# Kernel tuning notes

Hardware: AMD Instinct MI355X
Metric: run time of the kernel (lower is better)

## Reference

```python
import jax, jax.numpy as jnp
import numpy as np

B_, L_ = 8, 2048            # batch, seq_len
AD, VD, H = 512, 512, 256    # audio_dim, visual_dim, hidden_dim (= mamba d_model)
EXPAND, DSTATE, DCONV = 2, 16, 4
DIN = EXPAND * H             # mamba d_inner = 512
DTRANK = (H + 15) // 16      # ceil(d_model/16) = 16
NCLS = 8


def setup_inputs() -> dict:
    key = jax.random.key(0)
    ks = jax.random.split(key, 16)
    w = lambda k, shape, s=0.02: jax.random.normal(k, shape, jnp.float32) * s
    return {
        "audio_feats": jax.random.normal(ks[0], (B_, L_, AD), jnp.float32),
        "visual_feats": jax.random.normal(ks[1], (B_, L_, VD), jnp.float32),
        "audio_w": w(ks[2], (H, AD)), "audio_b": jnp.zeros((H,), jnp.float32),
        "visual_w": w(ks[3], (H, VD)), "visual_b": jnp.zeros((H,), jnp.float32),
        "q_w": w(ks[4], (H, H)), "q_b": jnp.zeros((H,), jnp.float32),
        "k_w": w(ks[5], (H, H)), "k_b": jnp.zeros((H,), jnp.float32),
        "v_w": w(ks[6], (H, H)), "v_b": jnp.zeros((H,), jnp.float32),
        "in_proj_w": w(ks[7], (2 * DIN, H)),
        "conv_w": w(ks[8], (DIN, DCONV), 0.1), "conv_b": jnp.zeros((DIN,), jnp.float32),
        "x_proj_w": w(ks[9], (DTRANK + 2 * DSTATE, DIN)),
        "dt_proj_w": w(ks[10], (DIN, DTRANK), 0.1),
        "dt_proj_b": jnp.full((DIN,), -4.0, jnp.float32),  # softplus(-4) ~ small dt
        "A_log": jnp.log(jnp.tile(jnp.arange(1, DSTATE + 1, dtype=jnp.float32), (DIN, 1))),
        "D": jnp.ones((DIN,), jnp.float32),
        "out_proj_w": w(ks[11], (H, DIN)),
        "cls_w": w(ks[12], (NCLS, H)), "cls_b": jnp.zeros((NCLS,), jnp.float32),
    }


def _linear(x, w, b):
    return jnp.einsum('...i,oi->...o', x, w) + b


def _mamba(u, in_proj_w, conv_w, conv_b, x_proj_w, dt_proj_w, dt_proj_b, A_log, D, out_proj_w):
    # u: [B, L, d_model]
    xz = jnp.einsum('bld,ed->ble', u, in_proj_w)          # [B, L, 2*DIN]
    x, z = jnp.split(xz, 2, axis=-1)
    # causal depthwise conv1d (torch pads d_conv-1 both sides then truncates to L)
    lhs = jnp.swapaxes(x, 1, 2)                            # [B, DIN, L]
    rhs = conv_w[:, None, :]                               # [DIN, 1, DCONV]
    xc = jax.lax.conv_general_dilated(lhs, rhs, (1,), [(DCONV - 1, 0)],
                                      feature_group_count=DIN)
    x = jax.nn.silu(jnp.swapaxes(xc, 1, 2) + conv_b)       # [B, L, DIN]
    dbc = jnp.einsum('bld,ed->ble', x, x_proj_w)           # [B, L, DTRANK+2*DSTATE]
    dt, Bm, Cm = jnp.split(dbc, [DTRANK, DTRANK + DSTATE], axis=-1)
    dt = jax.nn.softplus(jnp.einsum('blr,dr->bld', dt, dt_proj_w) + dt_proj_b)
    A = -jnp.exp(A_log)                                    # [DIN, DSTATE]

    def step(h, inputs):
        dt_t, B_t, C_t, x_t = inputs                       # [B,DIN],[B,DSTATE],[B,DSTATE],[B,DIN]
        dA = jnp.exp(dt_t[:, :, None] * A)                 # [B, DIN, DSTATE]
        h = dA * h + (dt_t * x_t)[:, :, None] * B_t[:, None, :]
        y = jnp.einsum('bds,bs->bd', h, C_t)
        return h, y

    h0 = jnp.zeros((u.shape[0], DIN, DSTATE), x.dtype)
    xs = (jnp.swapaxes(dt, 0, 1), jnp.swapaxes(Bm, 0, 1),
          jnp.swapaxes(Cm, 0, 1), jnp.swapaxes(x, 0, 1))
    _, ys = jax.lax.scan(step, h0, xs)                     # ys: [L, B, DIN]
    y = jnp.swapaxes(ys, 0, 1) + x * D
    y = y * jax.nn.silu(z)
    return jnp.einsum('bld,od->blo', y, out_proj_w)        # [B, L, d_model]


def reference(audio_feats, visual_feats, audio_w, audio_b, visual_w, visual_b,
              q_w, q_b, k_w, k_b, v_w, v_b, in_proj_w, conv_w, conv_b,
              x_proj_w, dt_proj_w, dt_proj_b, A_log, D, out_proj_w, cls_w, cls_b):
    ah = _linear(audio_feats, audio_w, audio_b)            # [B, L, H]
    vh = _linear(visual_feats, visual_w, visual_b)         # [B, L, H]
    Q = _linear(ah, q_w, q_b)
    K = _linear(vh, k_w, k_b)
    V = _linear(vh, v_w, v_b)
    scores = jnp.einsum('bqd,bkd->bqk', Q, K) / jnp.sqrt(jnp.float32(H))
    attn = jax.nn.softmax(scores, axis=-1)                 # [B, L, L]
    fused = jnp.einsum('bqk,bkd->bqd', attn, V)            # [B, L, H]
    mo = _mamba(fused, in_proj_w, conv_w, conv_b, x_proj_w,
                dt_proj_w, dt_proj_b, A_log, D, out_proj_w)
    pooled = mo.mean(axis=1)                               # [B, H]
    logits = _linear(pooled, cls_w, cls_b)                 # [B, NCLS]
    preds = jax.nn.softmax(logits, axis=-1)
    return logits, preds
```

## Files before the change

kernel.cpp:

```cpp
#include <hip/hip_runtime.h>
#include <hip/hip_bf16.h>
#include <math.h>

#define B_    8
#define L_    2048
#define AD    512
#define VD    512
#define H_    256
#define DIN   512
#define DSTATE 16
#define DCONV  4
#define DTRANK 16
#define NCLS   8
#define BL    (B_ * L_)
#define NCH   64
#define CLEN  32
#define NSP   4

typedef __attribute__((ext_vector_type(8))) short bf16x8;
typedef __attribute__((ext_vector_type(4))) float f32x4;

__global__ __launch_bounds__(256)
void cast_bf16_kernel(const float* __restrict__ src, __hip_bfloat16* __restrict__ dst)
{
    size_t i = ((size_t)blockIdx.x * 256 + threadIdx.x) * 8;
    float4 a = *(const float4*)(src + i);
    float4 b = *(const float4*)(src + i + 4);
    bf16x8 o;
    __hip_bfloat16 t;
    t = __float2bfloat16(a.x); o[0] = *(short*)&t;
    t = __float2bfloat16(a.y); o[1] = *(short*)&t;
    t = __float2bfloat16(a.z); o[2] = *(short*)&t;
    t = __float2bfloat16(a.w); o[3] = *(short*)&t;
    t = __float2bfloat16(b.x); o[4] = *(short*)&t;
    t = __float2bfloat16(b.y); o[5] = *(short*)&t;
    t = __float2bfloat16(b.z); o[6] = *(short*)&t;
    t = __float2bfloat16(b.w); o[7] = *(short*)&t;
    *(bf16x8*)(dst + i) = o;
}

__global__ __launch_bounds__(256)
void cast_weights_kernel(const float* __restrict__ qw, const float* __restrict__ kw,
                         const float* __restrict__ vw, const float* __restrict__ ipw,
                         const float* __restrict__ xpw,
                         __hip_bfloat16* __restrict__ qwb, __hip_bfloat16* __restrict__ kwb,
                         __hip_bfloat16* __restrict__ vwb, __hip_bfloat16* __restrict__ ipwb,
                         __hip_bfloat16* __restrict__ xpwb)
{
    size_t i = ((size_t)blockIdx.x * 256 + threadIdx.x) * 8;
    const float* s; __hip_bfloat16* d; size_t off;
    if      (i <  65536) { s = qw;  d = qwb;  off = i; }
    else if (i < 131072) { s = kw;  d = kwb;  off = i - 65536; }
    else if (i < 196608) { s = vw;  d = vwb;  off = i - 131072; }
    else if (i < 458752) { s = ipw; d = ipwb; off = i - 196608; }
    else                 { s = xpw; d = xpwb; off = i - 458752; }
    float4 a = *(const float4*)(s + off);
    float4 b = *(const float4*)(s + off + 4);
    bf16x8 o;
    __hip_bfloat16 t;
    t = __float2bfloat16(a.x); o[0] = *(short*)&t;
    t = __float2bfloat16(a.y); o[1] = *(short*)&t;
    t = __float2bfloat16(a.z); o[2] = *(short*)&t;
    t = __float2bfloat16(a.w); o[3] = *(short*)&t;
    t = __float2bfloat16(b.x); o[4] = *(short*)&t;
    t = __float2bfloat16(b.y); o[5] = *(short*)&t;
    t = __float2bfloat16(b.z); o[6] = *(short*)&t;
    t = __float2bfloat16(b.w); o[7] = *(short*)&t;
    *(bf16x8*)(d + off) = o;
}

__global__ __launch_bounds__(256)
void transpose_wT_kernel(const float* __restrict__ aw, const float* __restrict__ vw,
                         __hip_bfloat16* __restrict__ awT, __hip_bfloat16* __restrict__ vwT)
{
    int i = blockIdx.x * 256 + threadIdx.x;
    const float* s = (i < 131072) ? aw : vw;
    __hip_bfloat16* d = (i < 131072) ? awT : vwT;
    int j = i & 131071;
    int r = j >> 9;
    int c = j & 511;
    d[c * 256 + r] = __float2bfloat16(s[j]);
}

__global__ __launch_bounds__(256)
void bias_compose_kernel(const float* __restrict__ qw, const float* __restrict__ kw,
                         const float* __restrict__ vw,
                         const float* __restrict__ ab, const float* __restrict__ vb,
                         const float* __restrict__ qb, const float* __restrict__ kb,
                         const float* __restrict__ vb2,
                         float* __restrict__ bq, float* __restrict__ bkv)
{
    int m = threadIdx.x;
    int seg = blockIdx.x;
    const float* w  = (seg == 0) ? qw : (seg == 1) ? kw : vw;
    const float* ib = (seg == 0) ? ab : vb;
    const float* ob = (seg == 0) ? qb : (seg == 1) ? kb : vb2;
    float s = ob[m];
    for (int i = 0; i < 256; ++i) s += w[m * 256 + i] * ib[i];
    if (seg == 0) bq[m] = s;
    else          bkv[(seg - 1) * 256 + m] = s;
}

template<int N, int K, int OBF>
__global__ __launch_bounds__(64, 2)
void gemm_mfma_t(const __hip_bfloat16* __restrict__ A,
                 const __hip_bfloat16* __restrict__ W,
                 const float* __restrict__ bias,
                 void* __restrict__ outp)
{
    const int lane = threadIdx.x;
    const int l15  = lane & 15;
    const int quad = lane >> 4;
    const int m0   = blockIdx.x * 16;
    const int n0   = blockIdx.y * 64;

    const __hip_bfloat16* Arow = A + (size_t)(m0 + l15) * K + quad * 8;
    f32x4 acc[4];
    #pragma unroll
    for (int nt = 0; nt < 4; ++nt) acc[nt] = (f32x4){0.f, 0.f, 0.f, 0.f};

    #pragma unroll
    for (int kc = 0; kc < K; kc += 32) {
        bf16x8 af = *(const bf16x8*)(Arow + kc);
        #pragma unroll
        for (int nt = 0; nt < 4; ++nt) {
            bf16x8 bfv = *(const bf16x8*)(W + (size_t)(n0 + nt * 16 + l15) * K + kc + quad * 8);
            acc[nt] = __builtin_amdgcn_mfma_f32_16x16x32_bf16(af, bfv, acc[nt], 0, 0, 0);
        }
    }
    #pragma unroll
    for (int nt = 0; nt < 4; ++nt) {
        int col = n0 + nt * 16 + l15;
        float bv = bias ? bias[col] : 0.f;
        #pragma unroll
        for (int r = 0; r < 4; ++r) {
            size_t idx = (size_t)(m0 + quad * 4 + r) * N + col;
            float v = acc[nt][r] + bv;
            if (OBF) ((__hip_bfloat16*)outp)[idx] = __float2bfloat16(v);
            else     ((float*)outp)[idx] = v;
        }
    }
}

template<int N, int K, int NT, int OBF, int ACT>
__global__ __launch_bounds__(256, 2)
void gemm4_t(const __hip_bfloat16* __restrict__ A,
             const __hip_bfloat16* __restrict__ W,
             const float* __restrict__ bias,
             void* __restrict__ outp)
{
    constexpr int NROWS = NT * 16;
    __shared__ __attribute__((aligned(16))) short Ws[NROWS * 264];
    const int tid  = threadIdx.x;
    const int lane = tid & 63;
    const int w    = tid >> 6;
    const int l15  = lane & 15;
    const int quad = lane >> 4;
    const int m0   = blockIdx.x * 64 + w * 16;
    const int n0   = blockIdx.y * 64;

    constexpr int KC = K / 32;
    bf16x8 af[KC];
    const __hip_bfloat16* Arow = A + (size_t)(m0 + l15) * K + quad * 8;
    #pragma unroll
    for (int kc = 0; kc < KC; ++kc) af[kc] = *(const bf16x8*)(Arow + kc * 32);

    f32x4 acc[NT];
    #pragma unroll
    for (int nt = 0; nt < NT; ++nt) acc[nt] = (f32x4){0.f, 0.f, 0.f, 0.f};

    #pragma unroll
    for (int kh = 0; kh < K / 256; ++kh) {
        __syncthreads();
        #pragma unroll
        for (int i = 0; i < 8; ++i) {
            int id = tid + i * 256;
            int row = id >> 5, c = id & 31;
            if (row < NROWS)
                *(bf16x8*)&Ws[row * 264 + c * 8] =
                    *(const bf16x8*)(W + (size_t)(n0 + row) * K + kh * 256 + c * 8);
        }
        __syncthreads();
        #pragma unroll
        for (int kc = 0; kc < 8; ++kc) {
            #pragma unroll
            for (int nt = 0; nt < NT; ++nt) {
                bf16x8 wv = *(const bf16x8*)&Ws[(nt * 16 + l15) * 264 + kc * 32 + quad * 8];
                acc[nt] = __builtin_amdgcn_mfma_f32_16x16x32_bf16(af[kh * 8 + kc], wv, acc[nt], 0, 0, 0);
            }
        }
    }
    #pragma unroll
    for (int nt = 0; nt < NT; ++nt) {
        int col = n0 + nt * 16 + l15;
        float bv = bias ? bias[col] : 0.f;
        #pragma unroll
        for (int r = 0; r < 4; ++r) {
            size_t idx = (size_t)(m0 + quad * 4 + r) * N + col;
            float v = acc[nt][r] + bv;
            if (ACT) v = v / (1.f + __expf(-v));
            if (OBF) ((__hip_bfloat16*)outp)[idx] = __float2bfloat16(v);
            else     ((float*)outp)[idx] = v;
        }
    }
}

__global__ __launch_bounds__(256)
void transpose_v_kernel(const __hip_bfloat16* __restrict__ KV,
                        __hip_bfloat16* __restrict__ Vt)
{
    const int tid = threadIdx.x;
    const int lc  = blockIdx.x & 7;
    const int hg  = (blockIdx.x >> 3) & 31;
    const int b   = blockIdx.x >> 8;
    const int l   = lc * 256 + tid;
    bf16x8 v = *(const bf16x8*)(KV + ((size_t)b * L_ + l) * 512 + 256 + hg * 8);
    __hip_bfloat16* dst = Vt + (size_t)b * H_ * L_ + (size_t)(hg * 8) * L_ + l;
    #pragma unroll
    for (int j = 0; j < 8; ++j) {
        short s = v[j];
        dst[(size_t)j * L_] = *(__hip_bfloat16*)&s;
    }
}

__global__ __launch_bounds__(256, 3)
void attn_split_kernel(const __hip_bfloat16* __restrict__ Q,
                       const __hip_bfloat16* __restrict__ KV,
                       const __hip_bfloat16* __restrict__ Vt,
                       __hip_bfloat16* __restrict__ Opart,
                       float* __restrict__ lpart)
{
    __shared__ __attribute__((aligned(16))) short Ks[32 * 264];
    __shared__ __attribute__((aligned(16))) short Vs[256 * 40];
    __shared__ __attribute__((aligned(16))) short Pls[4][16 * 40];

    const int tid  = threadIdx.x;
    const int lane = tid & 63;
    const int w    = tid >> 6;
    const int b    = blockIdx.x & 7;
    const int qt   = (blockIdx.x >> 3) & 31;
    const int sp   = blockIdx.x >> 8;
    const int q0   = qt * 64 + w * 16;
    const int l15  = lane & 15;
    const int quad = lane >> 4;

    const __hip_bfloat16* Qb = Q  + ((size_t)b * L_ + q0) * H_;
    const __hip_bfloat16* Kb = KV + (size_t)b * L_ * 512;
    const __hip_bfloat16* Vb = Vt + (size_t)b * H_ * L_;

    bf16x8 qf[8];
    #pragma unroll
    for (int kc = 0; kc < 8; ++kc)
        qf[kc] = *(const bf16x8*)(Qb + (size_t)l15 * H_ + kc * 32 + quad * 8);

    f32x4 Oacc[16];
    #pragma unroll
    for (int nt = 0; nt < 16; ++nt) Oacc[nt] = (f32x4){0.f, 0.f, 0.f, 0.f};
    float lsum[4] = {0.f, 0.f, 0.f, 0.f};

    const int kbase = sp * 512;
    for (int st = 0; st < 16; ++st) {
        const int kb = kbase + st * 32;
        bf16x8 kreg[4], vreg[4];
        #pragma unroll
        for (int i = 0; i < 4; ++i) {
            int id = tid + i * 256;
            int row = id >> 5, c16 = id & 31;
            kreg[i] = *(const bf16x8*)(Kb + (size_t)(kb + row) * 512 + c16 * 8);
        }
        #pragma unroll
        for (int i = 0; i < 4; ++i) {
            int id = tid + i * 256;
            int row = id >> 2, c = id & 3;
            vreg[i] = *(const bf16x8*)(Vb + (size_t)row * L_ + kb + c * 8);
        }
        __syncthreads();
        #pragma unroll
        for (int i = 0; i < 4; ++i) {
            int id = tid + i * 256;
            int row = id >> 5, c16 = id & 31;
            *(bf16x8*)&Ks[row * 264 + c16 * 8] = kreg[i];
        }
        #pragma unroll
        for (int i = 0; i < 4; ++i) {
            int id = tid + i * 256;
            int row = id >> 2, c = id & 3;
            *(bf16x8*)&Vs[row * 40 + c * 8] = vreg[i];
        }
        __syncthreads();
        f32x4 S[2];
        #pragma unroll
        for (int nt = 0; nt < 2; ++nt) {
            S[nt] = (f32x4){0.f, 0.f, 0.f, 0.f};
            #pragma unroll
            for (int kc = 0; kc < 8; ++kc) {
                bf16x8 bk = *(const bf16x8*)&Ks[(nt * 16 + l15) * 264 + kc * 32 + quad * 8];
                S[nt] = __builtin_amdgcn_mfma_f32_16x16x32_bf16(qf[kc], bk, S[nt], 0, 0, 0);
            }
        }
        #pragma unroll
        for (int nt = 0; nt < 2; ++nt)
            #pragma unroll
            for (int r = 0; r < 4; ++r) {
                float p = __expf(S[nt][r] * 0.0625f);
                lsum[r] += p;
                __hip_bfloat16 pb = __float2bfloat16(p);
                Pls[w][(quad * 4 + r) * 40 + nt * 16 + l15] = *(short*)&pb;
            }
        bf16x8 pf = *(const bf16x8*)&Pls[w][l15 * 40 + quad * 8];
        #pragma unroll
        for (int nt = 0; nt < 16; ++nt) {
            bf16x8 vf = *(const bf16x8*)&Vs[(nt * 16 + l15) * 40 + quad * 8];
            Oacc[nt] = __builtin_amdgcn_mfma_f32_16x16x32_bf16(pf, vf, Oacc[nt], 0, 0, 0);
        }
    }
    #pragma unroll
    for (int r = 0; r < 4; ++r) {
        lsum[r] += __shfl_xor(lsum[r], 1, 64);
        lsum[r] += __shfl_xor(lsum[r], 2, 64);
        lsum[r] += __shfl_xor(lsum[r], 4, 64);
        lsum[r] += __shfl_xor(lsum[r], 8, 64);
    }
    __hip_bfloat16* Ob = Opart + (((size_t)sp * B_ + b) * L_ + q0) * H_;
    #pragma unroll
    for (int r = 0; r < 4; ++r)
        #pragma unroll
        for (int nt = 0; nt < 16; ++nt)
            Ob[(size_t)(quad * 4 + r) * H_ + nt * 16 + l15] = __float2bfloat16(Oacc[nt][r]);
    if (l15 == 0) {
        #pragma unroll
        for (int r = 0; r < 4; ++r)
            lpart[((size_t)sp * B_ + b) * L_ + q0 + quad * 4 + r] = lsum[r];
    }
}

__global__ __launch_bounds__(256)
void attn_merge_kernel(const __hip_bfloat16* __restrict__ Opart,
                       const float* __restrict__ lpart,
                       __hip_bfloat16* __restrict__ O)
{
    const size_t idx = (size_t)blockIdx.x * 256 + threadIdx.x;
    const size_t row = idx >> 8;
    float o = 0.f, l = 0.f;
    #pragma unroll
    for (int sp = 0; sp < NSP; ++sp) {
        o += __bfloat162float(Opart[(size_t)sp * BL * H_ + idx]);
        l += lpart[(size_t)sp * BL + row];
    }
    O[idx] = __float2bfloat16(o / l);
}

__global__ __launch_bounds__(256)
void conv_silu_kernel(const float* __restrict__ xb,
                      const float* __restrict__ cw,
                      const float* __restrict__ cb,
                      float* __restrict__ xconv,
                      __hip_bfloat16* __restrict__ xconvbf)
{
    const int idx = blockIdx.x * 256 + threadIdx.x;
    const int d = idx & (DIN - 1);
    const int l = (idx >> 9) & (L_ - 1);
    const int b = idx >> 20;
    float acc = cb[d];
    #pragma unroll
    for (int j = 0; j < DCONV; ++j) {
        int ls = l - (DCONV - 1) + j;
        if (ls >= 0) acc += xb[((size_t)b * L_ + ls) * DIN + d] * cw[d * DCONV + j];
    }
    float sg = 1.f / (1.f + __expf(-acc));
    float v = acc * sg;
    xconv[(size_t)idx] = v;
    xconvbf[(size_t)idx] = __float2bfloat16(v);
}

__global__ __launch_bounds__(256)
void scan_p1_kernel(const float* __restrict__ xconv,
                    const float* __restrict__ zw,
                    const float* __restrict__ dbc,
                    const float* __restrict__ dtw,
                    const float* __restrict__ dtbias,
                    const float* __restrict__ A_log,
                    const float* __restrict__ Dv,
                    float* __restrict__ hend,
                    float* __restrict__ aprod,
                    float* __restrict__ Gbuf,
                    float* __restrict__ accloc)
{
    __shared__ float Ds[CLEN][16];
    __shared__ float Bs[CLEN][16];
    __shared__ float Cs[CLEN][16];
    const int tid  = threadIdx.x;
    const int dgrp = blockIdx.x & 1;
    const int c    = (blockIdx.x >> 1) & 63;
    const int b    = blockIdx.x >> 7;
    const int d    = dgrp * 256 + tid;
    const size_t rbase = (size_t)b * L_ + c * CLEN;

    for (int i = tid; i < CLEN * 16; i += 256) {
        int tl = i >> 4, s = i & 15;
        Ds[tl][s] = dbc[(rbase + tl) * 48 + s];
        Bs[tl][s] = dbc[(rbase + tl) * 48 + 16 + s];
        Cs[tl][s] = dbc[(rbase + tl) * 48 + 32 + s];
    }
    __syncthreads();

    float wr[16];
    #pragma unroll
    for (int r = 0; r < 16; ++r) wr[r] = dtw[d * DTRANK + r];
    const float dbias = dtbias[d];
    const float Dval  = Dv[d];

    float Aa[16];
    bool fast = true;
    #pragma unroll
    for (int s = 0; s < 16; ++s) {
        Aa[s] = -__expf(A_log[d * DSTATE + s]);
        fast = fast && (fabsf(Aa[s] + (float)(s + 1)) < 1e-3f);
    }

    float h[16], ap[16], g[16];
    #pragma unroll
    for (int s = 0; s < 16; ++s) { h[s] = 0.f; ap[s] = 1.f; g[s] = 0.f; }
    float acc = 0.f;

    if (fast) {
        for (int t = 0; t < CLEN; ++t) {
            float d0 = dbias, d1 = 0.f;
            #pragma unroll
            for (int r = 0; r < 8; ++r) { d0 += Ds[t][r] * wr[r]; d1 += Ds[t][r + 8] * wr[r + 8]; }
            float dot = d0 + d1;
            float dtv = (dot > 20.f) ? dot : __logf(1.f + __expf(dot));
            float xv  = xconv[(rbase + t) * DIN + d];
            float wt  = zw   [(rbase + t) * DIN + d];
            float u  = dtv * xv;
            float e1 = __expf(-dtv);
            float ep = 1.f;
            #pragma unroll
            for (int s = 0; s < 16; ++s) {
                ep *= e1;
                ap[s] *= ep;
                h[s] = ep * h[s] + u * Bs[t][s];
                float tc = wt * Cs[t][s];
                acc += tc * h[s];
                g[s] += tc * ap[s];
            }
            acc += wt * xv * Dval;
        }
    } else {
        for (int t = 0; t < CLEN; ++t) {
            float d0 = dbias, d1 = 0.f;
            #pragma unroll
            for (int r = 0; r < 8; ++r) { d0 += Ds[t][r] * wr[r]; d1 += Ds[t][r + 8] * wr[r + 8]; }
            float dot = d0 + d1;
            float dtv = (dot > 20.f) ? dot : __logf(1.f + __expf(dot));
            float xv  = xconv[(rbase + t) * DIN + d];
            float wt  = zw   [(rbase + t) * DIN + d];
            float u  = dtv * xv;
            #pragma unroll
            for (int s = 0; s < 16; ++s) {
                float e = __expf(dtv * Aa[s]);
                ap[s] *= e;
                h[s] = e * h[s] + u * Bs[t][s];
                float tc = wt * Cs[t][s];
                acc += tc * h[s];
                g[s] += tc * ap[s];
            }
            acc += wt * xv * Dval;
        }
    }
    size_t o = (((size_t)b * NCH + c) * DIN + d) * 16;
    #pragma unroll
    for (int s = 0; s < 16; ++s) { hend[o + s] = h[s]; aprod[o + s] = ap[s]; Gbuf[o + s] = g[s]; }
    accloc[((size_t)b * NCH + c) * DIN + d] = acc;
}

__global__ __launch_bounds__(256)
void scan_p2_kernel(const float* __restrict__ hend,
                    const float* __restrict__ aprod,
                    const float* __restrict__ Gbuf,
                    const float* __restrict__ accloc,
                    float* __restrict__ ybar)
{
    const int g  = blockIdx.x * 256 + threadIdx.x;
    const int b  = g >> 13;
    const int ds = g & 8191;
    const int d  = ds >> 4;
    const int s  = ds & 15;
    float h = 0.f, part = 0.f;
    for (int c = 0; c < NCH; ++c) {
        size_t idx = (((size_t)b * NCH + c) << 13) + ds;
        part += Gbuf[idx] * h;
        h = aprod[idx] * h + hend[idx];
    }
    part += __shfl_xor(part, 1, 64);
    part += __shfl_xor(part, 2, 64);
    part += __shfl_xor(part, 4, 64);
    part += __shfl_xor(part, 8, 64);
    if (s == 0) {
        float a = 0.f;
        for (int c = 0; c < NCH; ++c)
            a += accloc[((size_t)b * NCH + c) * DIN + d];
        ybar[b * DIN + d] = (part + a) * (1.f / (float)L_);
    }
}

__global__ __launch_bounds__(256)
void head_kernel(const float* __restrict__ ybar,
                 const float* __restrict__ opw,
                 const float* __restrict__ clsw,
                 const float* __restrict__ clsb,
                 float* __restrict__ out)
{
    __shared__ float pooled_s[H_];
    __shared__ float logit_s[NCLS];
    const int tid = threadIdx.x;
    const int b   = blockIdx.x;
    const float* yb = ybar + b * DIN;
    const float* wr = opw + (size_t)tid * DIN;
    float p = 0.f;
    for (int dd = 0; dd < DIN; dd += 4) {
        float4 y4 = *(const float4*)(yb + dd);
        float4 w4 = *(const float4*)(wr + dd);
        p += y4.x*w4.x + y4.y*w4.y + y4.z*w4.z + y4.w*w4.w;
    }
    pooled_s[tid] = p;
    __syncthreads();
    if (tid < NCLS) {
        float lg = clsb[tid];
        const float* cw = clsw + tid * H_;
        for (int hh = 0; hh < H_; ++hh) lg += pooled_s[hh] * cw[hh];
        logit_s[tid] = lg;
        out[b * NCLS + tid] = lg;
    }
    __syncthreads();
    if (tid == 0) {
        float mx = logit_s[0];
        for (int c = 1; c < NCLS; ++c) mx = fmaxf(mx, logit_s[c]);
        float ssum = 0.f; float e[NCLS];
        for (int c = 0; c < NCLS; ++c) { e[c] = __expf(logit_s[c] - mx); ssum += e[c]; }
        for (int c = 0; c < NCLS; ++c) out[B_*NCLS + b * NCLS + c] = e[c] / ssum;
    }
}

extern "C" void kernel_launch(void* const* d_in, const int* in_sizes, int n_in,
                              void* d_out, int out_size, void* d_ws, size_t ws_size,
                              hipStream_t stream)
{
    const float* audio    = (const float*)d_in[0];
    const float* visual   = (const float*)d_in[1];
    const float* audio_w  = (const float*)d_in[2];
    const float* audio_b  = (const float*)d_in[3];
    const float* visual_w = (const float*)d_in[4];
    const float* visual_b = (const float*)d_in[5];
    const float* q_w = (const float*)d_in[6];
    const float* q_b = (const float*)d_in[7];
    const float* k_w = (const float*)d_in[8];
    const float* k_b = (const float*)d_in[9];
    const float* v_w = (const float*)d_in[10];
    const float* v_b = (const float*)d_in[11];
    const float* in_proj_w = (const float*)d_in[12];
    const float* conv_w    = (const float*)d_in[13];
    const float* conv_b    = (const float*)d_in[14];
    const float* x_proj_w  = (const float*)d_in[15];
    const float* dt_proj_w = (const float*)d_in[16];
    const float* dt_proj_b = (const float*)d_in[17];
    const float* A_log     = (const float*)d_in[18];
    const float* Dvec      = (const float*)d_in[19];
    const float* out_proj_w= (const float*)d_in[20];
    const float* cls_w     = (const float*)d_in[21];
    const float* cls_b     = (const float*)d_in[22];
    float* out = (float*)d_out;
    float* ws  = (float*)d_ws;

    __hip_bfloat16* abf  = (__hip_bfloat16*)(ws);
    __hip_bfloat16* vbf  = (__hip_bfloat16*)(ws + 4194304);
    __hip_bfloat16* Qbf  = (__hip_bfloat16*)(ws + 8388608);
    __hip_bfloat16* KVbf = (__hip_bfloat16*)(ws + 10485760);
    __hip_bfloat16* Vt   = (__hip_bfloat16*)(ws + 14680064);
    __hip_bfloat16* fusedbf = (__hip_bfloat16*)(ws + 16777216);
    __hip_bfloat16* Opart   = (__hip_bfloat16*)(ws + 18874368);
    float* xbuf  = ws;
    float* zw    = ws + 8388608;
    float* xconv = ws + 18874368;
    __hip_bfloat16* xconvbf = (__hip_bfloat16*)(ws + 27262976);
    float* hend   = ws;
    float* aprod  = ws + 4194304;
    float* Gbuf   = ws + 27262976;
    float* accloc = ws + 16777216;
    float* ybar   = ws + 17039360;
    __hip_bfloat16* q_wbf   = (__hip_bfloat16*)(ws + 31457280);
    __hip_bfloat16* k_wbf   = (__hip_bfloat16*)(ws + 31490048);
    __hip_bfloat16* v_wbf   = (__hip_bfloat16*)(ws + 31522816);
    __hip_bfloat16* ipwbf   = (__hip_bfloat16*)(ws + 31555584);
    __hip_bfloat16* xpwbf   = (__hip_bfloat16*)(ws + 31686656);
    __hip_bfloat16* awT     = (__hip_bfloat16*)(ws + 31698944);
    __hip_bfloat16* vwT     = (__hip_bfloat16*)(ws + 31764480);
    __hip_bfloat16* Wqp     = (__hip_bfloat16*)(ws + 31830016);
    __hip_bfloat16* Wkvp    = (__hip_bfloat16*)(ws + 31895552);
    float* bq     = ws + 32026624;
    float* bkv    = ws + 32026880;
    float* lpart  = ws + 32027392;
    float* dbcb   = ws + 32092928;

    dim3 blk(256);
    cast_bf16_kernel<<<dim3(4096), blk, 0, stream>>>(audio,  abf);
    cast_bf16_kernel<<<dim3(4096), blk, 0, stream>>>(visual, vbf);
    cast_weights_kernel<<<dim3(236), blk, 0, stream>>>(q_w, k_w, v_w, in_proj_w, x_proj_w,
                                                       q_wbf, k_wbf, v_wbf, ipwbf, xpwbf);
    transpose_wT_kernel<<<dim3(1024), blk, 0, stream>>>(audio_w, visual_w, awT, vwT);
    gemm_mfma_t<512, 256, 1><<<dim3(16, 8), dim3(64), 0, stream>>>(q_wbf, awT, nullptr, Wqp);
    gemm_mfma_t<512, 256, 1><<<dim3(16, 8), dim3(64), 0, stream>>>(k_wbf, vwT, nullptr, Wkvp);
    gemm_mfma_t<512, 256, 1><<<dim3(16, 8), dim3(64), 0, stream>>>(v_wbf, vwT, nullptr, Wkvp + 256 * 512);
    bias_compose_kernel<<<dim3(3), blk, 0, stream>>>(q_w, k_w, v_w, audio_b, visual_b,
                                                     q_b, k_b, v_b, bq, bkv);
    gemm4_t<256, 512, 4, 1, 0><<<dim3(256, 4), blk, 0, stream>>>(abf, Wqp,  bq,  Qbf);
    gemm4_t<512, 512, 4, 1, 0><<<dim3(256, 8), blk, 0, stream>>>(vbf, Wkvp, bkv, KVbf);
    transpose_v_kernel<<<dim3(2048), blk, 0, stream>>>(KVbf, Vt);
    attn_split_kernel<<<dim3(1024), blk, 0, stream>>>(Qbf, KVbf, Vt, Opart, lpart);
    attn_merge_kernel<<<dim3(16384), blk, 0, stream>>>(Opart, lpart, fusedbf);
    gemm4_t<512, 256, 4, 0, 0><<<dim3(256, 8), blk, 0, stream>>>(fusedbf, ipwbf,           nullptr, xbuf);
    gemm4_t<512, 256, 4, 0, 1><<<dim3(256, 8), blk, 0, stream>>>(fusedbf, ipwbf + DIN*H_,  nullptr, zw);
    conv_silu_kernel<<<dim3(BL*DIN/256), blk, 0, stream>>>(xbuf, conv_w, conv_b, xconv, xconvbf);
    gemm4_t<48, 512, 3, 0, 0><<<dim3(256, 1), blk, 0, stream>>>(xconvbf, xpwbf, nullptr, dbcb);
    scan_p1_kernel<<<dim3(1024), blk, 0, stream>>>(xconv, zw, dbcb, dt_proj_w, dt_proj_b,
                                                   A_log, Dvec, hend, aprod, Gbuf, accloc);
    scan_p2_kernel<<<dim3(256), blk, 0, stream>>>(hend, aprod, Gbuf, accloc, ybar);
    head_kernel<<<dim3(8), blk, 0, stream>>>(ybar, out_proj_w, cls_w, cls_b, out);
}
```

Measured before the change: 467.9 us.

## Merge prep kernels, widen attention tiles, store Mamba intermediates in bf16, split scan combine

Several independent changes. The input and weight cast, transpose and bias kernels are merged into fewer launches, and the three composition GEMMs now run as one 3D-grid launch. Attention blocks now cover 128 query rows, with each wave handling two 16-row sets so every K/V tile loaded into shared memory is reused twice; occupancy is lowered to 2 blocks. The in_proj outputs and conv output are stored as bf16 instead of fp32 to halve memory traffic, at some cost in precision. The sequential cross-chunk scan combine is split into two stages (groups of 8 chunks, then 8 groups) to expose more parallelism.

```diff
diff --git a/kernel.cpp b/kernel.cpp
--- a/kernel.cpp
+++ b/kernel.cpp
@@ -16,18 +16,14 @@
 #define NCH   64
 #define CLEN  32
 #define NSP   4
+#define NGRP  8
 
 typedef __attribute__((ext_vector_type(8))) short bf16x8;
 typedef __attribute__((ext_vector_type(4))) float f32x4;
 
-__global__ __launch_bounds__(256)
-void cast_bf16_kernel(const float* __restrict__ src, __hip_bfloat16* __restrict__ dst)
-{
-    size_t i = ((size_t)blockIdx.x * 256 + threadIdx.x) * 8;
-    float4 a = *(const float4*)(src + i);
-    float4 b = *(const float4*)(src + i + 4);
-    bf16x8 o;
-    __hip_bfloat16 t;
+__device__ inline bf16x8 pack8(float4 a, float4 b)
+{
+    bf16x8 o; __hip_bfloat16 t;
     t = __float2bfloat16(a.x); o[0] = *(short*)&t;
     t = __float2bfloat16(a.y); o[1] = *(short*)&t;
     t = __float2bfloat16(a.z); o[2] = *(short*)&t;
@@ -36,109 +32,108 @@
     t = __float2bfloat16(b.y); o[5] = *(short*)&t;
     t = __float2bfloat16(b.z); o[6] = *(short*)&t;
     t = __float2bfloat16(b.w); o[7] = *(short*)&t;
-    *(bf16x8*)(dst + i) = o;
-}
-
-__global__ __launch_bounds__(256)
-void cast_weights_kernel(const float* __restrict__ qw, const float* __restrict__ kw,
-                         const float* __restrict__ vw, const float* __restrict__ ipw,
-                         const float* __restrict__ xpw,
-                         __hip_bfloat16* __restrict__ qwb, __hip_bfloat16* __restrict__ kwb,
-                         __hip_bfloat16* __restrict__ vwb, __hip_bfloat16* __restrict__ ipwb,
-                         __hip_bfloat16* __restrict__ xpwb)
+    return o;
+}
+
+__global__ __launch_bounds__(256)
+void cast_inputs_kernel(const float* __restrict__ a, const float* __restrict__ v,
+                        __hip_bfloat16* __restrict__ ab, __hip_bfloat16* __restrict__ vb)
 {
     size_t i = ((size_t)blockIdx.x * 256 + threadIdx.x) * 8;
     const float* s; __hip_bfloat16* d; size_t off;
-    if      (i <  65536) { s = qw;  d = qwb;  off = i; }
-    else if (i < 131072) { s = kw;  d = kwb;  off = i - 65536; }
-    else if (i < 196608) { s = vw;  d = vwb;  off = i - 131072; }
-    else if (i < 458752) { s = ipw; d = ipwb; off = i - 196608; }
-    else                 { s = xpw; d = xpwb; off = i - 458752; }
-    float4 a = *(const float4*)(s + off);
-    float4 b = *(const float4*)(s + off + 4);
-    bf16x8 o;
-    __hip_bfloat16 t;
-    t = __float2bfloat16(a.x); o[0] = *(short*)&t;
-    t = __float2bfloat16(a.y); o[1] = *(short*)&t;
-    t = __float2bfloat16(a.z); o[2] = *(short*)&t;
-    t = __float2bfloat16(a.w); o[3] = *(short*)&t;
-    t = __float2bfloat16(b.x); o[4] = *(short*)&t;
-    t = __float2bfloat16(b.y); o[5] = *(short*)&t;
-    t = __float2bfloat16(b.z); o[6] = *(short*)&t;
-    t = __float2bfloat16(b.w); o[7] = *(short*)&t;
-    *(bf16x8*)(d + off) = o;
-}
-
-__global__ __launch_bounds__(256)
-void transpose_wT_kernel(const float* __restrict__ aw, const float* __restrict__ vw,
-                         __hip_bfloat16* __restrict__ awT, __hip_bfloat16* __restrict__ vwT)
-{
-    int i = blockIdx.x * 256 + threadIdx.x;
-    const float* s = (i < 131072) ? aw : vw;
-    __hip_bfloat16* d = (i < 131072) ? awT : vwT;
-    int j = i & 131071;
-    int r = j >> 9;
-    int c = j & 511;
-    d[c * 256 + r] = __float2bfloat16(s[j]);
-}
-
-__global__ __launch_bounds__(256)
-void bias_compose_kernel(const float* __restrict__ qw, const float* __restrict__ kw,
-                         const float* __restrict__ vw,
-                         const float* __restrict__ ab, const float* __restrict__ vb,
-                         const float* __restrict__ qb, const float* __restrict__ kb,
-                         const float* __restrict__ vb2,
-                         float* __restrict__ bq, float* __restrict__ bkv)
-{
-    int m = threadIdx.x;
-    int seg = blockIdx.x;
-    const float* w  = (seg == 0) ? qw : (seg == 1) ? kw : vw;
-    const float* ib = (seg == 0) ? ab : vb;
-    const float* ob = (seg == 0) ? qb : (seg == 1) ? kb : vb2;
-    float s = ob[m];
-    for (int i = 0; i < 256; ++i) s += w[m * 256 + i] * ib[i];
-    if (seg == 0) bq[m] = s;
-    else          bkv[(seg - 1) * 256 + m] = s;
-}
-
-template<int N, int K, int OBF>
+    if (i < 8388608) { s = a; d = ab; off = i; }
+    else             { s = v; d = vb; off = i - 8388608; }
+    float4 x = *(const float4*)(s + off);
+    float4 y = *(const float4*)(s + off + 4);
+    *(bf16x8*)(d + off) = pack8(x, y);
+}
+
+__global__ __launch_bounds__(256)
+void prep_kernel(const float* __restrict__ qw, const float* __restrict__ kw,
+                 const float* __restrict__ vw, const float* __restrict__ ipw,
+                 const float* __restrict__ xpw,
+                 const float* __restrict__ aw, const float* __restrict__ vww,
+                 const float* __restrict__ ab, const float* __restrict__ vb,
+                 const float* __restrict__ qb, const float* __restrict__ kb,
+                 const float* __restrict__ vb2,
+                 __hip_bfloat16* __restrict__ qwb, __hip_bfloat16* __restrict__ kwb,
+                 __hip_bfloat16* __restrict__ vwb, __hip_bfloat16* __restrict__ ipwb,
+                 __hip_bfloat16* __restrict__ xpwb,
+                 __hip_bfloat16* __restrict__ awT, __hip_bfloat16* __restrict__ vwT,
+                 float* __restrict__ bq, float* __restrict__ bkv)
+{
+    const int blk = blockIdx.x;
+    if (blk < 236) {
+        size_t i = ((size_t)blk * 256 + threadIdx.x) * 8;
+        const float* s; __hip_bfloat16* d; size_t off;
+        if      (i <  65536) { s = qw;  d = qwb;  off = i; }
+        else if (i < 131072) { s = kw;  d = kwb;  off = i - 65536; }
+        else if (i < 196608) { s = vw;  d = vwb;  off = i - 131072; }
+        else if (i < 458752) { s = ipw; d = ipwb; off = i - 196608; }
+        else                 { s = xpw; d = xpwb; off = i - 458752; }
+        float4 x = *(const float4*)(s + off);
+        float4 y = *(const float4*)(s + off + 4);
+        *(bf16x8*)(d + off) = pack8(x, y);
+    } else if (blk < 1260) {
+        int i = (blk - 236) * 256 + threadIdx.x;
+        const float* s = (i < 131072) ? aw : vww;
+        __hip_bfloat16* d = (i < 131072) ? awT : vwT;
+        int j = i & 131071;
+        int r = j >> 9, c = j & 511;
+        d[c * 256 + r] = __float2bfloat16(s[j]);
+    } else {
+        int seg = blk - 1260;
+        int m = threadIdx.x;
+        const float* w  = (seg == 0) ? qw : (seg == 1) ? kw : vw;
+        const float* ib = (seg == 0) ? ab : vb;
+        const float* ob = (seg == 0) ? qb : (seg == 1) ? kb : vb2;
+        float s = ob[m];
+        for (int i = 0; i < 256; ++i) s += w[m * 256 + i] * ib[i];
+        if (seg == 0) bq[m] = s;
+        else          bkv[(seg - 1) * 256 + m] = s;
+    }
+}
+
 __global__ __launch_bounds__(64, 2)
-void gemm_mfma_t(const __hip_bfloat16* __restrict__ A,
-                 const __hip_bfloat16* __restrict__ W,
-                 const float* __restrict__ bias,
-                 void* __restrict__ outp)
-{
+void gemm_comp_kernel(const __hip_bfloat16* __restrict__ qw,
+                      const __hip_bfloat16* __restrict__ kw,
+                      const __hip_bfloat16* __restrict__ vw,
+                      const __hip_bfloat16* __restrict__ awT,
+                      const __hip_bfloat16* __restrict__ vwT,
+                      __hip_bfloat16* __restrict__ Wqp,
+                      __hip_bfloat16* __restrict__ Wkvp)
+{
+    const int seg = blockIdx.z;
+    const __hip_bfloat16* A = (seg == 0) ? qw : (seg == 1) ? kw : vw;
+    const __hip_bfloat16* W = (seg == 0) ? awT : vwT;
+    __hip_bfloat16* outp = (seg == 0) ? Wqp : (Wkvp + (size_t)(seg - 1) * 256 * 512);
+
     const int lane = threadIdx.x;
     const int l15  = lane & 15;
     const int quad = lane >> 4;
     const int m0   = blockIdx.x * 16;
     const int n0   = blockIdx.y * 64;
 
-    const __hip_bfloat16* Arow = A + (size_t)(m0 + l15) * K + quad * 8;
+    const __hip_bfloat16* Arow = A + (size_t)(m0 + l15) * 256 + quad * 8;
     f32x4 acc[4];
     #pragma unroll
     for (int nt = 0; nt < 4; ++nt) acc[nt] = (f32x4){0.f, 0.f, 0.f, 0.f};
 
     #pragma unroll
-    for (int kc = 0; kc < K; kc += 32) {
+    for (int kc = 0; kc < 256; kc += 32) {
         bf16x8 af = *(const bf16x8*)(Arow + kc);
         #pragma unroll
         for (int nt = 0; nt < 4; ++nt) {
-            bf16x8 bfv = *(const bf16x8*)(W + (size_t)(n0 + nt * 16 + l15) * K + kc + quad * 8);
+            bf16x8 bfv = *(const bf16x8*)(W + (size_t)(n0 + nt * 16 + l15) * 256 + kc + quad * 8);
             acc[nt] = __builtin_amdgcn_mfma_f32_16x16x32_bf16(af, bfv, acc[nt], 0, 0, 0);
         }
     }
     #pragma unroll
     for (int nt = 0; nt < 4; ++nt) {
         int col = n0 + nt * 16 + l15;
-        float bv = bias ? bias[col] : 0.f;
-        #pragma unroll
-        for (int r = 0; r < 4; ++r) {
-            size_t idx = (size_t)(m0 + quad * 4 + r) * N + col;
-            float v = acc[nt][r] + bv;
-            if (OBF) ((__hip_bfloat16*)outp)[idx] = __float2bfloat16(v);
-            else     ((float*)outp)[idx] = v;
-        }
+        #pragma unroll
+        for (int r = 0; r < 4; ++r)
+            outp[(size_t)(m0 + quad * 4 + r) * 512 + col] = __float2bfloat16(acc[nt][r]);
     }
 }
 
@@ -223,7 +218,7 @@
     }
 }
 
-__global__ __launch_bounds__(256, 3)
+__global__ __launch_bounds__(256, 2)
 void attn_split_kernel(const __hip_bfloat16* __restrict__ Q,
                        const __hip_bfloat16* __restrict__ KV,
                        const __hip_bfloat16* __restrict__ Vt,
@@ -232,15 +227,15 @@
 {
     __shared__ __attribute__((aligned(16))) short Ks[32 * 264];
     __shared__ __attribute__((aligned(16))) short Vs[256 * 40];
-    __shared__ __attribute__((aligned(16))) short Pls[4][16 * 40];
+    __shared__ __attribute__((aligned(16))) short Pls[4][2][16 * 40];
 
     const int tid  = threadIdx.x;
     const int lane = tid & 63;
     const int w    = tid >> 6;
     const int b    = blockIdx.x & 7;
-    const int qt   = (blockIdx.x >> 3) & 31;
-    const int sp   = blockIdx.x >> 8;
-    const int q0   = qt * 64 + w * 16;
+    const int qt   = (blockIdx.x >> 3) & 15;
+    const int sp   = blockIdx.x >> 7;
+    const int q0   = qt * 128 + w * 32;
     const int l15  = lane & 15;
     const int quad = lane >> 4;
 
@@ -248,15 +243,19 @@
     const __hip_bfloat16* Kb = KV + (size_t)b * L_ * 512;
     const __hip_bfloat16* Vb = Vt + (size_t)b * H_ * L_;
 
-    bf16x8 qf[8];
-    #pragma unroll
-    for (int kc = 0; kc < 8; ++kc)
-        qf[kc] = *(const bf16x8*)(Qb + (size_t)l15 * H_ + kc * 32 + quad * 8);
-
-    f32x4 Oacc[16];
-    #pragma unroll
-    for (int nt = 0; nt < 16; ++nt) Oacc[nt] = (f32x4){0.f, 0.f, 0.f, 0.f};
-    float lsum[4] = {0.f, 0.f, 0.f, 0.f};
+    bf16x8 qf[2][8];
+    #pragma unroll
+    for (int s2 = 0; s2 < 2; ++s2)
+        #pragma unroll
+        for (int kc = 0; kc < 8; ++kc)
+            qf[s2][kc] = *(const bf16x8*)(Qb + (size_t)(s2 * 16 + l15) * H_ + kc * 32 + quad * 8);
+
+    f32x4 Oacc[2][16];
+    #pragma unroll
+    for (int s2 = 0; s2 < 2; ++s2)
+        #pragma unroll
+        for (int nt = 0; nt < 16; ++nt) Oacc[s2][nt] = (f32x4){0.f, 0.f, 0.f, 0.f};
+    float lsum[2][4] = {{0.f,0.f,0.f,0.f},{0.f,0.f,0.f,0.f}};
 
     const int kbase = sp * 512;
     for (int st = 0; st < 16; ++st) {
@@ -288,49 +287,61 @@
             *(bf16x8*)&Vs[row * 40 + c * 8] = vreg[i];
         }
         __syncthreads();
-        f32x4 S[2];
         #pragma unroll
         for (int nt = 0; nt < 2; ++nt) {
-            S[nt] = (f32x4){0.f, 0.f, 0.f, 0.f};
+            f32x4 S0 = (f32x4){0.f,0.f,0.f,0.f};
+            f32x4 S1 = (f32x4){0.f,0.f,0.f,0.f};
             #pragma unroll
             for (int kc = 0; kc < 8; ++kc) {
                 bf16x8 bk = *(const bf16x8*)&Ks[(nt * 16 + l15) * 264 + kc * 32 + quad * 8];
-                S[nt] = __builtin_amdgcn_mfma_f32_16x16x32_bf16(qf[kc], bk, S[nt], 0, 0, 0);
+                S0 = __builtin_amdgcn_mfma_f32_16x16x32_bf16(qf[0][kc], bk, S0, 0, 0, 0);
+                S1 = __builtin_amdgcn_mfma_f32_16x16x32_bf16(qf[1][kc], bk, S1, 0, 0, 0);
             }
-        }
-        #pragma unroll
-        for (int nt = 0; nt < 2; ++nt)
             #pragma unroll
             for (int r = 0; r < 4; ++r) {
-                float p = __expf(S[nt][r] * 0.0625f);
-                lsum[r] += p;
-                __hip_bfloat16 pb = __float2bfloat16(p);
-                Pls[w][(quad * 4 + r) * 40 + nt * 16 + l15] = *(short*)&pb;
+                float p0 = __expf(S0[r] * 0.0625f);
+                float p1 = __expf(S1[r] * 0.0625f);
+                lsum[0][r] += p0;
+                lsum[1][r] += p1;
+                __hip_bfloat16 pb0 = __float2bfloat16(p0);
+                __hip_bfloat16 pb1 = __float2bfloat16(p1);
+                Pls[w][0][(quad * 4 + r) * 40 + nt * 16 + l15] = *(short*)&pb0;
+                Pls[w][1][(quad * 4 + r) * 40 + nt * 16 + l15] = *(short*)&pb1;
             }
-        bf16x8 pf = *(const bf16x8*)&Pls[w][l15 * 40 + quad * 8];
+        }
+        bf16x8 pf0 = *(const bf16x8*)&Pls[w][0][l15 * 40 + quad * 8];
+        bf16x8 pf1 = *(const bf16x8*)&Pls[w][1][l15 * 40 + quad * 8];
         #pragma unroll
         for (int nt = 0; nt < 16; ++nt) {
             bf16x8 vf = *(const bf16x8*)&Vs[(nt * 16 + l15) * 40 + quad * 8];
-            Oacc[nt] = __builtin_amdgcn_mfma_f32_16x16x32_bf16(pf, vf, Oacc[nt], 0, 0, 0);
-        }
-    }
-    #pragma unroll
-    for (int r = 0; r < 4; ++r) {
-        lsum[r] += __shfl_xor(lsum[r], 1, 64);
-        lsum[r] += __shfl_xor(lsum[r], 2, 64);
-        lsum[r] += __shfl_xor(lsum[r], 4, 64);
-        lsum[r] += __shfl_xor(lsum[r], 8, 64);
-    }
+            Oacc[0][nt] = __builtin_amdgcn_mfma_f32_16x16x32_bf16(pf0, vf, Oacc[0][nt], 0, 0, 0);
+            Oacc[1][nt] = __builtin_amdgcn_mfma_f32_16x16x32_bf16(pf1, vf, Oacc[1][nt], 0, 0, 0);
+        }
+    }
+    #pragma unroll
+    for (int s2 = 0; s2 < 2; ++s2)
+        #pragma unroll
+        for (int r = 0; r < 4; ++r) {
+            lsum[s2][r] += __shfl_xor(lsum[s2][r], 1, 64);
+            lsum[s2][r] += __shfl_xor(lsum[s2][r], 2, 64);
+            lsum[s2][r] += __shfl_xor(lsum[s2][r], 4, 64);
+            lsum[s2][r] += __shfl_xor(lsum[s2][r], 8, 64);
+        }
     __hip_bfloat16* Ob = Opart + (((size_t)sp * B_ + b) * L_ + q0) * H_;
     #pragma unroll
-    for (int r = 0; r < 4; ++r)
-        #pragma unroll
-        for (int nt = 0; nt < 16; ++nt)
-            Ob[(size_t)(quad * 4 + r) * H_ + nt * 16 + l15] = __float2bfloat16(Oacc[nt][r]);
+    for (int s2 = 0; s2 < 2; ++s2)
+        #pragma unroll
+        for (int r = 0; r < 4; ++r)
+            #pragma unroll
+            for (int nt = 0; nt < 16; ++nt)
+                Ob[(size_t)(s2 * 16 + quad * 4 + r) * H_ + nt * 16 + l15] =
+                    __float2bfloat16(Oacc[s2][nt][r]);
     if (l15 == 0) {
         #pragma unroll
-        for (int r = 0; r < 4; ++r)
-            lpart[((size_t)sp * B_ + b) * L_ + q0 + quad * 4 + r] = lsum[r];
+        for (int s2 = 0; s2 < 2; ++s2)
+            #pragma unroll
+            for (int r = 0; r < 4; ++r)
+                lpart[((size_t)sp * B_ + b) * L_ + q0 + s2 * 16 + quad * 4 + r] = lsum[s2][r];
     }
 }
 
@@ -351,10 +362,9 @@
 }
 
 __global__ __launch_bounds__(256)
-void conv_silu_kernel(const float* __restrict__ xb,
+void conv_silu_kernel(const __hip_bfloat16* __restrict__ xb,
                       const float* __restrict__ cw,
                       const float* __restrict__ cb,
-                      float* __restrict__ xconv,
                       __hip_bfloat16* __restrict__ xconvbf)
 {
     const int idx = blockIdx.x * 256 + threadIdx.x;
@@ -365,17 +375,16 @@
     #pragma unroll
     for (int j = 0; j < DCONV; ++j) {
         int ls = l - (DCONV - 1) + j;
-        if (ls >= 0) acc += xb[((size_t)b * L_ + ls) * DIN + d] * cw[d * DCONV + j];
+        if (ls >= 0)
+            acc += __bfloat162float(xb[((size_t)b * L_ + ls) * DIN + d]) * cw[d * DCONV + j];
     }
     float sg = 1.f / (1.f + __expf(-acc));
-    float v = acc * sg;
-    xconv[(size_t)idx] = v;
-    xconvbf[(size_t)idx] = __float2bfloat16(v);
-}
-
-__global__ __launch_bounds__(256)
-void scan_p1_kernel(const float* __restrict__ xconv,
-                    const float* __restrict__ zw,
+    xconvbf[(size_t)idx] = __float2bfloat16(acc * sg);
+}
+
+__global__ __launch_bounds__(256)
+void scan_p1_kernel(const __hip_bfloat16* __restrict__ xconv,
+                    const __hip_bfloat16* __restrict__ zw,
                     const float* __restrict__ dbc,
                     const float* __restrict__ dtw,
                     const float* __restrict__ dtbias,
@@ -430,8 +439,8 @@
             for (int r = 0; r < 8; ++r) { d0 += Ds[t][r] * wr[r]; d1 += Ds[t][r + 8] * wr[r + 8]; }
             float dot = d0 + d1;
             float dtv = (dot > 20.f) ? dot : __logf(1.f + __expf(dot));
-            float xv  = xconv[(rbase + t) * DIN + d];
-            float wt  = zw   [(rbase + t) * DIN + d];
+            float xv  = __bfloat162float(xconv[(rbase + t) * DIN + d]);
+            float wt  = __bfloat162float(zw   [(rbase + t) * DIN + d]);
             float u  = dtv * xv;
             float e1 = __expf(-dtv);
             float ep = 1.f;
@@ -453,8 +462,8 @@
             for (int r = 0; r < 8; ++r) { d0 += Ds[t][r] * wr[r]; d1 += Ds[t][r + 8] * wr[r + 8]; }
             float dot = d0 + d1;
             float dtv = (dot > 20.f) ? dot : __logf(1.f + __expf(dot));
-            float xv  = xconv[(rbase + t) * DIN + d];
-            float wt  = zw   [(rbase + t) * DIN + d];
+            float xv  = __bfloat162float(xconv[(rbase + t) * DIN + d]);
+            float wt  = __bfloat162float(zw   [(rbase + t) * DIN + d]);
             float u  = dtv * xv;
             #pragma unroll
             for (int s = 0; s < 16; ++s) {
@@ -475,11 +484,45 @@
 }
 
 __global__ __launch_bounds__(256)
-void scan_p2_kernel(const float* __restrict__ hend,
-                    const float* __restrict__ aprod,
-                    const float* __restrict__ Gbuf,
-                    const float* __restrict__ accloc,
-                    float* __restrict__ ybar)
+void scan_p2a_kernel(const float* __restrict__ hend,
+                     const float* __restrict__ aprod,
+                     const float* __restrict__ Gbuf,
+                     const float* __restrict__ accloc,
+                     float* __restrict__ hg, float* __restrict__ Pg,
+                     float* __restrict__ Wg, float* __restrict__ part0g,
+                     float* __restrict__ accg)
+{
+    const int g   = blockIdx.x * 256 + threadIdx.x;
+    const int b   = g >> 16;
+    const int grp = (g >> 13) & 7;
+    const int ds  = g & 8191;
+    float h = 0.f, P = 1.f, W = 0.f, p0 = 0.f;
+    #pragma unroll
+    for (int j = 0; j < 8; ++j) {
+        int c = grp * 8 + j;
+        size_t idx = (((size_t)b * NCH + c) << 13) + ds;
+        float G = Gbuf[idx], ap = aprod[idx], he = hend[idx];
+        p0 += G * h;
+        W  += G * P;
+        h   = ap * h + he;
+        P  *= ap;
+    }
+    size_t o = (((size_t)b * NGRP + grp) << 13) + ds;
+    hg[o] = h; Pg[o] = P; Wg[o] = W; part0g[o] = p0;
+    if (ds < DIN) {
+        float a = 0.f;
+        #pragma unroll
+        for (int j = 0; j < 8; ++j)
+            a += accloc[((size_t)b * NCH + grp * 8 + j) * DIN + ds];
+        accg[((size_t)b * NGRP + grp) * DIN + ds] = a;
+    }
+}
+
+__global__ __launch_bounds__(256)
+void scan_p2b_kernel(const float* __restrict__ hg, const float* __restrict__ Pg,
+                     const float* __restrict__ Wg, const float* __restrict__ part0g,
+                     const float* __restrict__ accg,
+                     float* __restrict__ ybar)
 {
     const int g  = blockIdx.x * 256 + threadIdx.x;
     const int b  = g >> 13;
@@ -487,10 +530,11 @@
     const int d  = ds >> 4;
     const int s  = ds & 15;
     float h = 0.f, part = 0.f;
-    for (int c = 0; c < NCH; ++c) {
-        size_t idx = (((size_t)b * NCH + c) << 13) + ds;
-        part += Gbuf[idx] * h;
-        h = aprod[idx] * h + hend[idx];
+    #pragma unroll
+    for (int grp = 0; grp < NGRP; ++grp) {
+        size_t o = (((size_t)b * NGRP + grp) << 13) + ds;
+        part += part0g[o] + Wg[o] * h;
+        h = Pg[o] * h + hg[o];
     }
     part += __shfl_xor(part, 1, 64);
     part += __shfl_xor(part, 2, 64);
@@ -498,8 +542,9 @@
     part += __shfl_xor(part, 8, 64);
     if (s == 0) {
         float a = 0.f;
-        for (int c = 0; c < NCH; ++c)
-            a += accloc[((size_t)b * NCH + c) * DIN + d];
+        #pragma unroll
+        for (int grp = 0; grp < NGRP; ++grp)
+            a += accg[((size_t)b * NGRP + grp) * DIN + d];
         ybar[b * DIN + d] = (part + a) * (1.f / (float)L_);
     }
 }
@@ -579,15 +624,16 @@
     __hip_bfloat16* Vt   = (__hip_bfloat16*)(ws + 14680064);
     __hip_bfloat16* fusedbf = (__hip_bfloat16*)(ws + 16777216);
     __hip_bfloat16* Opart   = (__hip_bfloat16*)(ws + 18874368);
-    float* xbuf  = ws;
-    float* zw    = ws + 8388608;
-    float* xconv = ws + 18874368;
     __hip_bfloat16* xconvbf = (__hip_bfloat16*)(ws + 27262976);
+    __hip_bfloat16* xbufbf = (__hip_bfloat16*)(ws);
+    __hip_bfloat16* zwbf   = (__hip_bfloat16*)(ws + 4194304);
     float* hend   = ws;
-    float* aprod  = ws + 4194304;
-    float* Gbuf   = ws + 27262976;
-    float* accloc = ws + 16777216;
-    float* ybar   = ws + 17039360;
+    float* Gbuf   = ws + 18874368;
+    float* aprod  = ws + 23068672;
+    float* hg     = ws + 16777216;
+    float* Pg     = ws + 17301504;
+    float* Wgb    = ws + 17825792;
+    float* part0g = ws + 18350080;
     __hip_bfloat16* q_wbf   = (__hip_bfloat16*)(ws + 31457280);
     __hip_bfloat16* k_wbf   = (__hip_bfloat16*)(ws + 31490048);
     __hip_bfloat16* v_wbf   = (__hip_bfloat16*)(ws + 31522816);
@@ -601,29 +647,31 @@
     float* bkv    = ws + 32026880;
     float* lpart  = ws + 32027392;
     float* dbcb   = ws + 32092928;
+    float* accloc = ws + 32879360;
+    float* accg   = ws + 33141504;
+    float* ybar   = ws + 33174272;
 
     dim3 blk(256);
-    cast_bf16_kernel<<<dim3(4096), blk, 0, stream>>>(audio,  abf);
-    cast_bf16_kernel<<<dim3(4096), blk, 0, stream>>>(visual, vbf);
-    cast_weights_kernel<<<dim3(236), blk, 0, stream>>>(q_w, k_w, v_w, in_proj_w, x_proj_w,
-                                                       q_wbf, k_wbf, v_wbf, ipwbf, xpwbf);
-    transpose_wT_kernel<<<dim3(1024), blk, 0, stream>>>(audio_w, visual_w, awT, vwT);
-    gemm_mfma_t<512, 256, 1><<<dim3(16, 8), dim3(64), 0, stream>>>(q_wbf, awT, nullptr, Wqp);
-    gemm_mfma_t<512, 256, 1><<<dim3(16, 8), dim3(64), 0, stream>>>(k_wbf, vwT, nullptr, Wkvp);
-    gemm_mfma_t<512, 256, 1><<<dim3(16, 8), dim3(64), 0, stream>>>(v_wbf, vwT, nullptr, Wkvp + 256 * 512);
-    bias_compose_kernel<<<dim3(3), blk, 0, stream>>>(q_w, k_w, v_w, audio_b, visual_b,
-                                                     q_b, k_b, v_b, bq, bkv);
+    cast_inputs_kernel<<<dim3(8192), blk, 0, stream>>>(audio, visual, abf, vbf);
+    prep_kernel<<<dim3(1263), blk, 0, stream>>>(q_w, k_w, v_w, in_proj_w, x_proj_w,
+                                                audio_w, visual_w, audio_b, visual_b,
+                                                q_b, k_b, v_b,
+                                                q_wbf, k_wbf, v_wbf, ipwbf, xpwbf,
+                                                awT, vwT, bq, bkv);
+    gemm_comp_kernel<<<dim3(16, 8, 3), dim3(64), 0, stream>>>(q_wbf, k_wbf, v_wbf, awT, vwT, Wqp, Wkvp);
     gemm4_t<256, 512, 4, 1, 0><<<dim3(256, 4), blk, 0, stream>>>(abf, Wqp,  bq,  Qbf);
     gemm4_t<512, 512, 4, 1, 0><<<dim3(256, 8), blk, 0, stream>>>(vbf, Wkvp, bkv, KVbf);
     transpose_v_kernel<<<dim3(2048), blk, 0, stream>>>(KVbf, Vt);
-    attn_split_kernel<<<dim3(1024), blk, 0, stream>>>(Qbf, KVbf, Vt, Opart, lpart);
+    attn_split_kernel<<<dim3(512), blk, 0, stream>>>(Qbf, KVbf, Vt, Opart, lpart);
     attn_merge_kernel<<<dim3(16384), blk, 0, stream>>>(Opart, lpart, fusedbf);
-    gemm4_t<512, 256, 4, 0, 0><<<dim3(256, 8), blk, 0, stream>>>(fusedbf, ipwbf,           nullptr, xbuf);
-    gemm4_t<512, 256, 4, 0, 1><<<dim3(256, 8), blk, 0, stream>>>(fusedbf, ipwbf + DIN*H_,  nullptr, zw);
-    conv_silu_kernel<<<dim3(BL*DIN/256), blk, 0, stream>>>(xbuf, conv_w, conv_b, xconv, xconvbf);
+    gemm4_t<512, 256, 4, 1, 0><<<dim3(256, 8), blk, 0, stream>>>(fusedbf, ipwbf,           nullptr, xbufbf);
+    gemm4_t<512, 256, 4, 1, 1><<<dim3(256, 8), blk, 0, stream>>>(fusedbf, ipwbf + DIN*H_,  nullptr, zwbf);
+    conv_silu_kernel<<<dim3(BL*DIN/256), blk, 0, stream>>>(xbufbf, conv_w, conv_b, xconvbf);
     gemm4_t<48, 512, 3, 0, 0><<<dim3(256, 1), blk, 0, stream>>>(xconvbf, xpwbf, nullptr, dbcb);
-    scan_p1_kernel<<<dim3(1024), blk, 0, stream>>>(xconv, zw, dbcb, dt_proj_w, dt_proj_b,
+    scan_p1_kernel<<<dim3(1024), blk, 0, stream>>>(xconvbf, zwbf, dbcb, dt_proj_w, dt_proj_b,
                                                    A_log, Dvec, hend, aprod, Gbuf, accloc);
-    scan_p2_kernel<<<dim3(256), blk, 0, stream>>>(hend, aprod, Gbuf, accloc, ybar);
+    scan_p2a_kernel<<<dim3(2048), blk, 0, stream>>>(hend, aprod, Gbuf, accloc,
+                                                    hg, Pg, Wgb, part0g, accg);
+    scan_p2b_kernel<<<dim3(256), blk, 0, stream>>>(hg, Pg, Wgb, part0g, accg, ybar);
     head_kernel<<<dim3(8), blk, 0, stream>>>(ybar, out_proj_w, cls_w, cls_b, out);
 }
```

Measured after the change: 455.6 us. -2.6%, faster.
